# Kernel optimization log

Measured on AMD Instinct MI355X. Metric: run time of the kernel, lower is better.

The kernel has to match this reference:

```python
import jax, jax.numpy as jnp
import numpy as np

ALPHA = 0.2  # LeakyReLU negative slope
NEG_INF = -9e15


def setup_inputs() -> dict:
    key = jax.random.key(0)
    k1, k2, k3, k4 = jax.random.split(key, 4)
    B, S, N, F_in, F_out = 4, 8, 1024, 128, 64
    inputs = jax.random.normal(k1, (B, S, N, F_in), dtype=jnp.float32)
    Adj = jax.random.randint(k2, (B, S, N, N), 0, 2, dtype=jnp.int32)
    # xavier_normal_ with gain=1.414
    W = jax.random.normal(k3, (F_in, F_out), dtype=jnp.float32) * np.float32(1.414 * np.sqrt(2.0 / (F_in + F_out)))
    a = jax.random.normal(k4, (2 * F_out, 1), dtype=jnp.float32) * np.float32(1.414 * np.sqrt(2.0 / (2 * F_out + 1)))
    return {"inputs": inputs, "Adj": Adj, "W": W, "a": a}


def reference(inputs, Adj, W, a):
    h = jnp.einsum('bsnf,fo->bsno', inputs, W)  # [B,S,N,F_out]
    F_out = h.shape[-1]
    # additive score e_ij = leakyrelu(a1.h_i + a2.h_j); identical math to the
    # original concat([h_i, h_j]) @ a without the O(N^2 * 2F) tensor.
    a1 = a[:F_out, 0]
    a2 = a[F_out:, 0]
    f1 = h @ a1  # [B,S,N]
    f2 = h @ a2  # [B,S,N]
    e = jax.nn.leaky_relu(f1[..., :, None] + f2[..., None, :], ALPHA)  # [B,S,N,N]
    att = jnp.where(Adj > 0, e, jnp.float32(NEG_INF))
    att = jax.nn.softmax(att, axis=1)  # faithful to original: softmax over dim=1 (SEQ)
    # dropout omitted (p=0.0 / eval mode)
    h_prime = jnp.matmul(att, h)  # [B,S,N,F_out]
    return jax.nn.elu(h_prime), Adj  # concat=True branch
```

## Files before the change

### kernel.cpp

```cpp
#include <hip/hip_runtime.h>
#include <cstdint>
#include <cstddef>

#define LALPHA 0.2f
#define NEG_INF -9000000000000000.0f

constexpr int N_ = 1024;
constexpr int FIN = 128, FO = 64;
constexpr int BS = 32;
constexpr size_t H_ELEMS = (size_t)BS * N_ * FO;
constexpr size_t F_ELEMS = (size_t)BS * N_;
constexpr int SPLITK = 8;

typedef __attribute__((ext_vector_type(8))) short short8;
typedef __attribute__((ext_vector_type(4))) float floatx4;

static __device__ __forceinline__ unsigned short f2bf(float x) {
    union { float f; unsigned u; } v; v.f = x;
    unsigned r = v.u + 0x7FFF + ((v.u >> 16) & 1);
    return (unsigned short)(r >> 16);
}
static __device__ __forceinline__ float bf2f_lo(unsigned u) {
    union { unsigned u; float f; } v; v.u = u << 16; return v.f;
}
static __device__ __forceinline__ float bf2f_hi(unsigned u) {
    union { unsigned u; float f; } v; v.u = u & 0xFFFF0000u; return v.f;
}

__global__ __launch_bounds__(256) void k_h(
    const float* __restrict__ x, const float* __restrict__ W,
    const float* __restrict__ a, float* __restrict__ h,
    float* __restrict__ f1, float* __restrict__ f2)
{
    __shared__ float sW[FIN * FO];
    __shared__ float sx[4][FIN];
    const int t = threadIdx.x;
    for (int i = t; i < FIN * FO; i += 256) sW[i] = W[i];
    const size_t node0 = (size_t)blockIdx.x * 4;
    for (int i = t; i < 4 * FIN; i += 256) sx[i >> 7][i & 127] = x[node0 * FIN + i];
    __syncthreads();

    const int wave = t >> 6;
    const int lane = t & 63;
    const size_t node = node0 + wave;

    float acc = 0.f;
    #pragma unroll
    for (int f = 0; f < FIN; ++f)
        acc = fmaf(sx[wave][f], sW[f * FO + lane], acc);

    h[node * FO + lane] = acc;

    float v1 = acc * a[lane];
    float v2 = acc * a[FO + lane];
    #pragma unroll
    for (int off = 32; off > 0; off >>= 1) {
        v1 += __shfl_xor(v1, off);
        v2 += __shfl_xor(v2, off);
    }
    if (lane == 0) { f1[node] = v1; f2[node] = v2; }
}

__global__ __launch_bounds__(256) void k_tr(
    const float* __restrict__ h, unsigned short* __restrict__ hT)
{
    __shared__ float lt[64][65];
    const int bs = blockIdx.x >> 4;
    const int n0 = (blockIdx.x & 15) * 64;
    const int t = threadIdx.x;
    const float* hb = h + ((size_t)bs << 16) + ((size_t)n0 << 6);
    #pragma unroll
    for (int k = 0; k < 4; ++k) {
        const int r = (t >> 4) + k * 16;
        const int c = (t & 15) * 4;
        const float4 v = *(const float4*)(hb + ((size_t)r << 6) + c);
        lt[r][c] = v.x; lt[r][c + 1] = v.y; lt[r][c + 2] = v.z; lt[r][c + 3] = v.w;
    }
    __syncthreads();
    const int o = t >> 2, ch = (t & 3) * 16;
    unsigned short tmp[16];
    #pragma unroll
    for (int q = 0; q < 16; ++q) tmp[q] = f2bf(lt[ch + q][o]);
    unsigned short* dst = hT + ((size_t)bs << 16) + ((size_t)o << 10) + n0 + ch;
    *(uint4*)dst = *(uint4*)tmp;
    *(uint4*)(dst + 8) = *(uint4*)(tmp + 8);
}

__global__ __launch_bounds__(256, 4) void k_av(
    const int* __restrict__ Adj, const float* __restrict__ f1,
    const float* __restrict__ f2, const unsigned short* __restrict__ hT,
    unsigned short* __restrict__ part, float* __restrict__ out_adj)
{
    __shared__ __align__(16) unsigned short att[8][16][64];

    const int bid   = blockIdx.x;
    const int kk    = bid >> 8;
    const int b     = (bid >> 6) & 3;
    const int i0    = (bid & 63) * 16;
    const int t     = threadIdx.x;

    const int p_jj = (t & 15) * 4;
    const int p_ii = t >> 4;
    const int gi   = i0 + p_ii;

    const int w  = t >> 6;
    const int l  = t & 63;
    const int fr = l & 15;
    const int fg = l >> 4;

    float fi[8];
    #pragma unroll
    for (int s = 0; s < 8; ++s) fi[s] = f1[(size_t)(b * 8 + s) * N_ + gi];

    floatx4 acc[2][4];
    #pragma unroll
    for (int si = 0; si < 2; ++si)
        #pragma unroll
        for (int n = 0; n < 4; ++n)
            acc[si][n] = (floatx4){0.f, 0.f, 0.f, 0.f};

    for (int jt = 0; jt < 2; ++jt) {
        const int j0 = (kk * 2 + jt) * 64;

        int4 ad[8];
        #pragma unroll
        for (int s = 0; s < 8; ++s) {
            const size_t aoff = ((size_t)(b * 8 + s) << 20) + ((size_t)gi << 10) + (size_t)(j0 + p_jj);
            ad[s] = *(const int4*)(Adj + aoff);
        }
        float ev[8][4];
        #pragma unroll
        for (int s = 0; s < 8; ++s) {
            const size_t aoff = ((size_t)(b * 8 + s) << 20) + ((size_t)gi << 10) + (size_t)(j0 + p_jj);
            *(float4*)(out_adj + aoff) =
                make_float4((float)ad[s].x, (float)ad[s].y, (float)ad[s].z, (float)ad[s].w);
            const float4 fj = *(const float4*)(f2 + (size_t)(b * 8 + s) * N_ + j0 + p_jj);
            const float v0 = fi[s] + fj.x, v1 = fi[s] + fj.y;
            const float v2 = fi[s] + fj.z, v3 = fi[s] + fj.w;
            ev[s][0] = ad[s].x > 0 ? (v0 >= 0.f ? v0 : LALPHA * v0) : NEG_INF;
            ev[s][1] = ad[s].y > 0 ? (v1 >= 0.f ? v1 : LALPHA * v1) : NEG_INF;
            ev[s][2] = ad[s].z > 0 ? (v2 >= 0.f ? v2 : LALPHA * v2) : NEG_INF;
            ev[s][3] = ad[s].w > 0 ? (v3 >= 0.f ? v3 : LALPHA * v3) : NEG_INF;
        }
        #pragma unroll
        for (int q = 0; q < 4; ++q) {
            float m = NEG_INF;
            #pragma unroll
            for (int s = 0; s < 8; ++s) m = fmaxf(m, ev[s][q]);
            float p[8], den = 0.f;
            #pragma unroll
            for (int s = 0; s < 8; ++s) { p[s] = __expf(ev[s][q] - m); den += p[s]; }
            const float r = 1.0f / den;
            #pragma unroll
            for (int s = 0; s < 8; ++s) ev[s][q] = p[s] * r;
        }
        {
            const int chs  = (p_jj >> 3) ^ (p_ii & 7);
            const int boff = chs * 16 + (p_jj & 7) * 2;
            #pragma unroll
            for (int s = 0; s < 8; ++s) {
                ushort4 wv;
                wv.x = f2bf(ev[s][0]); wv.y = f2bf(ev[s][1]);
                wv.z = f2bf(ev[s][2]); wv.w = f2bf(ev[s][3]);
                *(ushort4*)((char*)&att[s][p_ii][0] + boff) = wv;
            }
        }
        __syncthreads();

        #pragma unroll
        for (int ks = 0; ks < 2; ++ks) {
            short8 af[2];
            #pragma unroll
            for (int si = 0; si < 2; ++si) {
                const int s = 2 * w + si;
                const int c = (ks * 4 + fg) ^ (fr & 7);
                af[si] = *(const short8*)((const char*)&att[s][fr][0] + c * 16);
            }
            #pragma unroll
            for (int n = 0; n < 4; ++n) {
                #pragma unroll
                for (int si = 0; si < 2; ++si) {
                    const int bs = b * 8 + 2 * w + si;
                    const short8 bf = *(const short8*)(
                        hT + ((size_t)bs << 16) + (size_t)(n * 16 + fr) * N_ + j0 + ks * 32 + fg * 8);
                    acc[si][n] = __builtin_amdgcn_mfma_f32_16x16x32_bf16(af[si], bf, acc[si][n], 0, 0, 0);
                }
            }
        }
        __syncthreads();
    }

    #pragma unroll
    for (int si = 0; si < 2; ++si) {
        const int bs = b * 8 + 2 * w + si;
        #pragma unroll
        for (int n = 0; n < 4; ++n) {
            #pragma unroll
            for (int r = 0; r < 4; ++r) {
                part[(size_t)kk * H_ELEMS + ((size_t)bs << 16)
                     + (size_t)(i0 + fg * 4 + r) * FO + n * 16 + fr] = f2bf(acc[si][n][r]);
            }
        }
    }
}

__global__ __launch_bounds__(256) void k_comb(
    const unsigned short* __restrict__ part, float* __restrict__ out_h)
{
    const size_t idx = ((size_t)blockIdx.x * 256 + threadIdx.x) * 8;
    float acc[8] = {0.f,0.f,0.f,0.f,0.f,0.f,0.f,0.f};
    #pragma unroll
    for (int p = 0; p < SPLITK; ++p) {
        const uint4 v = *(const uint4*)(part + (size_t)p * H_ELEMS + idx);
        acc[0] += bf2f_lo(v.x); acc[1] += bf2f_hi(v.x);
        acc[2] += bf2f_lo(v.y); acc[3] += bf2f_hi(v.y);
        acc[4] += bf2f_lo(v.z); acc[5] += bf2f_hi(v.z);
        acc[6] += bf2f_lo(v.w); acc[7] += bf2f_hi(v.w);
    }
    float4 r0, r1;
    r0.x = acc[0] > 0.f ? acc[0] : expm1f(acc[0]);
    r0.y = acc[1] > 0.f ? acc[1] : expm1f(acc[1]);
    r0.z = acc[2] > 0.f ? acc[2] : expm1f(acc[2]);
    r0.w = acc[3] > 0.f ? acc[3] : expm1f(acc[3]);
    r1.x = acc[4] > 0.f ? acc[4] : expm1f(acc[4]);
    r1.y = acc[5] > 0.f ? acc[5] : expm1f(acc[5]);
    r1.z = acc[6] > 0.f ? acc[6] : expm1f(acc[6]);
    r1.w = acc[7] > 0.f ? acc[7] : expm1f(acc[7]);
    *(float4*)(out_h + idx) = r0;
    *(float4*)(out_h + idx + 4) = r1;
}

extern "C" void kernel_launch(void* const* d_in, const int* in_sizes, int n_in,
                              void* d_out, int out_size, void* d_ws, size_t ws_size,
                              hipStream_t stream)
{
    const float* x   = (const float*)d_in[0];
    const int*   Adj = (const int*)d_in[1];
    const float* W   = (const float*)d_in[2];
    const float* a   = (const float*)d_in[3];

    float* out = (float*)d_out;
    float* ws  = (float*)d_ws;

    float* f1 = ws;
    float* f2 = f1 + F_ELEMS;
    unsigned short* hT = (unsigned short*)(f2 + F_ELEMS);
    float* h = f2 + F_ELEMS + H_ELEMS / 2;
    unsigned short* part = (unsigned short*)h;

    float* out_h   = out;
    float* out_adj = out + H_ELEMS;

    hipLaunchKernelGGL(k_h,    dim3(BS * N_ / 4),           dim3(256), 0, stream, x, W, a, h, f1, f2);
    hipLaunchKernelGGL(k_tr,   dim3(BS * 16),               dim3(256), 0, stream, h, hT);
    hipLaunchKernelGGL(k_av,   dim3(SPLITK * 4 * 64),       dim3(256), 0, stream, Adj, f1, f2, hT, part, out_adj);
    hipLaunchKernelGGL(k_comb, dim3((int)(H_ELEMS / 2048)), dim3(256), 0, stream, part, out_h);
}
```

Before: 153.6 us.

## Split adjacency conversion into a packing kernel emitting per-seq bitmasks

Adds a separate k_pack kernel that reads the int32 adjacency once, writes the float copy to the output, and packs the 8 sequence-axis mask bits per (b,i,j) into one byte. The attention kernel then reads a 4-byte packed word instead of eight int4 loads and no longer writes the adjacency output. This aims to shrink the memory traffic and register pressure in k_av. It costs an extra launch and a 4 MB packed buffer round-trip through workspace, while total Adj read/write traffic stays the same.

```diff
diff --git a/kernel.cpp b/kernel.cpp
--- a/kernel.cpp
+++ b/kernel.cpp
@@ -86,10 +86,37 @@
     *(uint4*)(dst + 8) = *(uint4*)(tmp + 8);
 }
 
+__global__ __launch_bounds__(256) void k_pack(
+    const int* __restrict__ Adj, float* __restrict__ adjf,
+    unsigned char* __restrict__ packed)
+{
+    const size_t tid = (size_t)blockIdx.x * 256 + threadIdx.x;
+    const int j4 = (int)(tid & 255) * 4;
+    const int i  = (int)((tid >> 8) & 1023);
+    const int b  = (int)(tid >> 18);
+
+    unsigned b0 = 0, b1 = 0, b2 = 0, b3 = 0;
+    #pragma unroll
+    for (int s = 0; s < 8; ++s) {
+        const size_t off = ((size_t)(b * 8 + s) << 20) + ((size_t)i << 10) + (size_t)j4;
+        const int4 ad = *(const int4*)(Adj + off);
+        *(float4*)(adjf + off) =
+            make_float4((float)ad.x, (float)ad.y, (float)ad.z, (float)ad.w);
+        b0 |= (unsigned)(ad.x > 0) << s;
+        b1 |= (unsigned)(ad.y > 0) << s;
+        b2 |= (unsigned)(ad.z > 0) << s;
+        b3 |= (unsigned)(ad.w > 0) << s;
+    }
+    uchar4 pk;
+    pk.x = (unsigned char)b0; pk.y = (unsigned char)b1;
+    pk.z = (unsigned char)b2; pk.w = (unsigned char)b3;
+    *(uchar4*)(packed + ((size_t)b << 20) + ((size_t)i << 10) + (size_t)j4) = pk;
+}
+
 __global__ __launch_bounds__(256, 4) void k_av(
-    const int* __restrict__ Adj, const float* __restrict__ f1,
+    const unsigned char* __restrict__ packed, const float* __restrict__ f1,
     const float* __restrict__ f2, const unsigned short* __restrict__ hT,
-    unsigned short* __restrict__ part, float* __restrict__ out_adj)
+    unsigned short* __restrict__ part)
 {
     __shared__ __align__(16) unsigned short att[8][16][64];
 
@@ -122,25 +149,20 @@
     for (int jt = 0; jt < 2; ++jt) {
         const int j0 = (kk * 2 + jt) * 64;
 
-        int4 ad[8];
+        const uchar4 pk = *(const uchar4*)(
+            packed + ((size_t)b << 20) + ((size_t)gi << 10) + (size_t)(j0 + p_jj));
+        const unsigned bq0 = pk.x, bq1 = pk.y, bq2 = pk.z, bq3 = pk.w;
+
+        float ev[8][4];
         #pragma unroll
         for (int s = 0; s < 8; ++s) {
-            const size_t aoff = ((size_t)(b * 8 + s) << 20) + ((size_t)gi << 10) + (size_t)(j0 + p_jj);
-            ad[s] = *(const int4*)(Adj + aoff);
-        }
-        float ev[8][4];
-        #pragma unroll
-        for (int s = 0; s < 8; ++s) {
-            const size_t aoff = ((size_t)(b * 8 + s) << 20) + ((size_t)gi << 10) + (size_t)(j0 + p_jj);
-            *(float4*)(out_adj + aoff) =
-                make_float4((float)ad[s].x, (float)ad[s].y, (float)ad[s].z, (float)ad[s].w);
             const float4 fj = *(const float4*)(f2 + (size_t)(b * 8 + s) * N_ + j0 + p_jj);
             const float v0 = fi[s] + fj.x, v1 = fi[s] + fj.y;
             const float v2 = fi[s] + fj.z, v3 = fi[s] + fj.w;
-            ev[s][0] = ad[s].x > 0 ? (v0 >= 0.f ? v0 : LALPHA * v0) : NEG_INF;
-            ev[s][1] = ad[s].y > 0 ? (v1 >= 0.f ? v1 : LALPHA * v1) : NEG_INF;
-            ev[s][2] = ad[s].z > 0 ? (v2 >= 0.f ? v2 : LALPHA * v2) : NEG_INF;
-            ev[s][3] = ad[s].w > 0 ? (v3 >= 0.f ? v3 : LALPHA * v3) : NEG_INF;
+            ev[s][0] = (bq0 >> s) & 1 ? (v0 >= 0.f ? v0 : LALPHA * v0) : NEG_INF;
+            ev[s][1] = (bq1 >> s) & 1 ? (v1 >= 0.f ? v1 : LALPHA * v1) : NEG_INF;
+            ev[s][2] = (bq2 >> s) & 1 ? (v2 >= 0.f ? v2 : LALPHA * v2) : NEG_INF;
+            ev[s][3] = (bq3 >> s) & 1 ? (v3 >= 0.f ? v3 : LALPHA * v3) : NEG_INF;
         }
         #pragma unroll
         for (int q = 0; q < 4; ++q) {
@@ -245,7 +267,8 @@
     float* f1 = ws;
     float* f2 = f1 + F_ELEMS;
     unsigned short* hT = (unsigned short*)(f2 + F_ELEMS);
-    float* h = f2 + F_ELEMS + H_ELEMS / 2;
+    unsigned char* packed = (unsigned char*)(hT + H_ELEMS);
+    float* h = (float*)(packed + (size_t)4 * 1024 * 1024);
     unsigned short* part = (unsigned short*)h;
 
     float* out_h   = out;
@@ -253,6 +276,7 @@
 
     hipLaunchKernelGGL(k_h,    dim3(BS * N_ / 4),           dim3(256), 0, stream, x, W, a, h, f1, f2);
     hipLaunchKernelGGL(k_tr,   dim3(BS * 16),               dim3(256), 0, stream, h, hT);
-    hipLaunchKernelGGL(k_av,   dim3(SPLITK * 4 * 64),       dim3(256), 0, stream, Adj, f1, f2, hT, part, out_adj);
+    hipLaunchKernelGGL(k_pack, dim3(4096),                  dim3(256), 0, stream, Adj, out_adj, packed);
+    hipLaunchKernelGGL(k_av,   dim3(SPLITK * 4 * 64),       dim3(256), 0, stream, packed, f1, f2, hT, part);
     hipLaunchKernelGGL(k_comb, dim3((int)(H_ELEMS / 2048)), dim3(256), 0, stream, part, out_h);
 }
```

Result: no change. 154.6 us (+0.7%).

## Double-buffer attention tiles and overlap Adj loads with MFMA, halve split-K

Applied to the files above, without the earlier changes.

The attention-times-h kernel now handles four 64-column j-tiles per block instead of two, halving split-K and therefore the partial buffer traffic and the combine work. It double-buffers the shared attention tile so that the Adj loads and softmax for the next tile are issued while MFMAs run on the current one, with raised wave priority around the MFMA section. Nontemporal loads and stores are used for streaming Adj, out_adj, the partials and the output. The trade-offs are fewer blocks (less parallelism), more shared memory per block, and higher register pressure from keeping Adj loads in flight.

```diff
diff --git a/kernel.cpp b/kernel.cpp
--- a/kernel.cpp
+++ b/kernel.cpp
@@ -10,10 +10,12 @@
 constexpr int BS = 32;
 constexpr size_t H_ELEMS = (size_t)BS * N_ * FO;
 constexpr size_t F_ELEMS = (size_t)BS * N_;
-constexpr int SPLITK = 8;
+constexpr int SPLITK = 4;
 
 typedef __attribute__((ext_vector_type(8))) short short8;
 typedef __attribute__((ext_vector_type(4))) float floatx4;
+typedef __attribute__((ext_vector_type(4))) int   i32x4;
+typedef __attribute__((ext_vector_type(4))) unsigned u32x4;
 
 static __device__ __forceinline__ unsigned short f2bf(float x) {
     union { float f; unsigned u; } v; v.f = x;
@@ -91,7 +93,7 @@
     const float* __restrict__ f2, const unsigned short* __restrict__ hT,
     unsigned short* __restrict__ part, float* __restrict__ out_adj)
 {
-    __shared__ __align__(16) unsigned short att[8][16][64];
+    __shared__ __align__(16) unsigned short att[2][8][16][64];
 
     const int bid   = blockIdx.x;
     const int kk    = bid >> 8;
@@ -119,21 +121,27 @@
         for (int n = 0; n < 4; ++n)
             acc[si][n] = (floatx4){0.f, 0.f, 0.f, 0.f};
 
-    for (int jt = 0; jt < 2; ++jt) {
-        const int j0 = (kk * 2 + jt) * 64;
-
-        int4 ad[8];
+    i32x4 ad[8];
+
+    auto issue_loads = [&](int jt) {
+        const int j0 = (kk * 4 + jt) * 64;
         #pragma unroll
         for (int s = 0; s < 8; ++s) {
             const size_t aoff = ((size_t)(b * 8 + s) << 20) + ((size_t)gi << 10) + (size_t)(j0 + p_jj);
-            ad[s] = *(const int4*)(Adj + aoff);
-        }
+            ad[s] = __builtin_nontemporal_load((const i32x4*)(Adj + aoff));
+        }
+    };
+
+    auto softmax_store = [&](int jt, int pb) {
+        const int j0 = (kk * 4 + jt) * 64;
         float ev[8][4];
         #pragma unroll
         for (int s = 0; s < 8; ++s) {
             const size_t aoff = ((size_t)(b * 8 + s) << 20) + ((size_t)gi << 10) + (size_t)(j0 + p_jj);
-            *(float4*)(out_adj + aoff) =
-                make_float4((float)ad[s].x, (float)ad[s].y, (float)ad[s].z, (float)ad[s].w);
+            floatx4 o;
+            o.x = (float)ad[s].x; o.y = (float)ad[s].y;
+            o.z = (float)ad[s].z; o.w = (float)ad[s].w;
+            __builtin_nontemporal_store(o, (floatx4*)(out_adj + aoff));
             const float4 fj = *(const float4*)(f2 + (size_t)(b * 8 + s) * N_ + j0 + p_jj);
             const float v0 = fi[s] + fj.x, v1 = fi[s] + fj.y;
             const float v2 = fi[s] + fj.z, v3 = fi[s] + fj.w;
@@ -154,19 +162,20 @@
             #pragma unroll
             for (int s = 0; s < 8; ++s) ev[s][q] = p[s] * r;
         }
-        {
-            const int chs  = (p_jj >> 3) ^ (p_ii & 7);
-            const int boff = chs * 16 + (p_jj & 7) * 2;
-            #pragma unroll
-            for (int s = 0; s < 8; ++s) {
-                ushort4 wv;
-                wv.x = f2bf(ev[s][0]); wv.y = f2bf(ev[s][1]);
-                wv.z = f2bf(ev[s][2]); wv.w = f2bf(ev[s][3]);
-                *(ushort4*)((char*)&att[s][p_ii][0] + boff) = wv;
-            }
-        }
-        __syncthreads();
-
+        const int chs  = (p_jj >> 3) ^ (p_ii & 7);
+        const int boff = chs * 16 + (p_jj & 7) * 2;
+        #pragma unroll
+        for (int s = 0; s < 8; ++s) {
+            ushort4 wv;
+            wv.x = f2bf(ev[s][0]); wv.y = f2bf(ev[s][1]);
+            wv.z = f2bf(ev[s][2]); wv.w = f2bf(ev[s][3]);
+            *(ushort4*)((char*)&att[pb][s][p_ii][0] + boff) = wv;
+        }
+    };
+
+    auto do_mfma = [&](int jt, int pb) {
+        const int j0 = (kk * 4 + jt) * 64;
+        __builtin_amdgcn_s_setprio(1);
         #pragma unroll
         for (int ks = 0; ks < 2; ++ks) {
             short8 af[2];
@@ -174,7 +183,7 @@
             for (int si = 0; si < 2; ++si) {
                 const int s = 2 * w + si;
                 const int c = (ks * 4 + fg) ^ (fr & 7);
-                af[si] = *(const short8*)((const char*)&att[s][fr][0] + c * 16);
+                af[si] = *(const short8*)((const char*)&att[pb][s][fr][0] + c * 16);
             }
             #pragma unroll
             for (int n = 0; n < 4; ++n) {
@@ -187,8 +196,20 @@
                 }
             }
         }
+        __builtin_amdgcn_s_setprio(0);
+    };
+
+    issue_loads(0);
+    softmax_store(0, 0);
+    __syncthreads();
+    #pragma unroll
+    for (int jt = 1; jt < 4; ++jt) {
+        issue_loads(jt);
+        do_mfma(jt - 1, (jt - 1) & 1);
+        softmax_store(jt, jt & 1);
         __syncthreads();
     }
+    do_mfma(3, 1);
 
     #pragma unroll
     for (int si = 0; si < 2; ++si) {
@@ -197,8 +218,9 @@
         for (int n = 0; n < 4; ++n) {
             #pragma unroll
             for (int r = 0; r < 4; ++r) {
-                part[(size_t)kk * H_ELEMS + ((size_t)bs << 16)
-                     + (size_t)(i0 + fg * 4 + r) * FO + n * 16 + fr] = f2bf(acc[si][n][r]);
+                __builtin_nontemporal_store(f2bf(acc[si][n][r]),
+                    part + (size_t)kk * H_ELEMS + ((size_t)bs << 16)
+                         + (size_t)(i0 + fg * 4 + r) * FO + n * 16 + fr);
             }
         }
     }
@@ -211,13 +233,14 @@
     float acc[8] = {0.f,0.f,0.f,0.f,0.f,0.f,0.f,0.f};
     #pragma unroll
     for (int p = 0; p < SPLITK; ++p) {
-        const uint4 v = *(const uint4*)(part + (size_t)p * H_ELEMS + idx);
+        const u32x4 v = __builtin_nontemporal_load(
+            (const u32x4*)(part + (size_t)p * H_ELEMS + idx));
         acc[0] += bf2f_lo(v.x); acc[1] += bf2f_hi(v.x);
         acc[2] += bf2f_lo(v.y); acc[3] += bf2f_hi(v.y);
         acc[4] += bf2f_lo(v.z); acc[5] += bf2f_hi(v.z);
         acc[6] += bf2f_lo(v.w); acc[7] += bf2f_hi(v.w);
     }
-    float4 r0, r1;
+    floatx4 r0, r1;
     r0.x = acc[0] > 0.f ? acc[0] : expm1f(acc[0]);
     r0.y = acc[1] > 0.f ? acc[1] : expm1f(acc[1]);
     r0.z = acc[2] > 0.f ? acc[2] : expm1f(acc[2]);
@@ -226,8 +249,8 @@
     r1.y = acc[5] > 0.f ? acc[5] : expm1f(acc[5]);
     r1.z = acc[6] > 0.f ? acc[6] : expm1f(acc[6]);
     r1.w = acc[7] > 0.f ? acc[7] : expm1f(acc[7]);
-    *(float4*)(out_h + idx) = r0;
-    *(float4*)(out_h + idx + 4) = r1;
+    __builtin_nontemporal_store(r0, (floatx4*)(out_h + idx));
+    __builtin_nontemporal_store(r1, (floatx4*)(out_h + idx + 4));
 }
 
 extern "C" void kernel_launch(void* const* d_in, const int* in_sizes, int n_in,
@@ -245,7 +268,7 @@
     float* f1 = ws;
     float* f2 = f1 + F_ELEMS;
     unsigned short* hT = (unsigned short*)(f2 + F_ELEMS);
-    float* h = f2 + F_ELEMS + H_ELEMS / 2;
+    float* h = (float*)(hT + H_ELEMS);
     unsigned short* part = (unsigned short*)h;
 
     float* out_h   = out;
```

Result: slower. 174.4 us (+13.5%).
